# Kernel tuning notes

Measured on AMD Instinct MI355X. Metric: run time of the kernel, lower is better.

The kernel has to match this reference:

```python
import jax, jax.numpy as jnp
import numpy as np

B, S, V, H, K, T = 4, 256, 32000, 1024, 4, 20
THRESHOLD = 0.6


def setup_inputs() -> dict:
    key = jax.random.key(0)
    ks = jax.random.split(key, 12)
    sH = 1.0 / np.sqrt(H)
    return {
        "input_ids": jax.random.randint(ks[0], (B, S), 0, V),
        "labels": jax.random.randint(ks[1], (B, S), 0, V),
        "embed": jax.random.normal(ks[2], (V, H), jnp.float32) * 0.02,
        "W1": jax.random.normal(ks[3], (H, H), jnp.float32) * sH,
        "b1": jnp.zeros((H,), jnp.float32),
        "lm_head": jax.random.normal(ks[4], (H, V), jnp.float32) * 0.02,
        "W_gen": jax.random.normal(ks[5], (H, H), jnp.float32) * sH,
        "thought_emb": jax.random.normal(ks[6], (K, H), jnp.float32) * 0.02,
        "tpos_emb": jax.random.normal(ks[7], (T, H), jnp.float32) * 0.02,
        "w_score": jax.random.normal(ks[8], (2 * H,), jnp.float32) * sH,
        "w_gate": jax.random.normal(ks[9], (2 * H,), jnp.float32) * sH,
    }


def reference(input_ids, labels, embed, W1, b1, lm_head, W_gen,
              thought_emb, tpos_emb, w_score, w_gate):
    # ---- base model: embed -> tanh MLP -> lm_head ----
    h0 = embed[input_ids]                                 # (B,S,H)
    hidden = jnp.tanh(h0 @ W1 + b1)                       # base last_hidden_state
    base_logits = hidden @ lm_head                        # (B,S,V)

    # ---- ThoughtInjector: per-position gate from normalized entropy ----
    logp = jax.nn.log_softmax(base_logits, axis=-1)
    ent = -jnp.sum(jnp.exp(logp) * logp, axis=-1) / jnp.log(float(V))  # (B,S)
    inject = (ent.mean(axis=0) > THRESHOLD) & (jnp.arange(S) < S - 1)   # (S,)

    # ---- ThoughtGenerator: (B,S,K,T,H) thoughts (masked dispatch, all pos) ----
    g = jnp.tanh(hidden @ W_gen)                          # (B,S,H)
    thoughts = jnp.tanh(g[:, :, None, None, :]
                        + thought_emb[None, None, :, None, :]
                        + tpos_emb[None, None, None, :, :])  # (B,S,K,T,H)
    tmean = thoughts.mean(axis=3)                         # (B,S,K,H) = thoughts.mean(dim=2)

    # ---- CoherenceScorer: composite score per thought ----
    comp = jax.nn.sigmoid(
        jnp.einsum('bsh,h->bs', hidden, w_score[:H])[:, :, None]
        + jnp.einsum('bskh,h->bsk', tmean, w_score[H:]))  # (B,S,K)

    # ---- MixingHead: coherence-weighted thought mix, gated blend with hidden ----
    alpha = jax.nn.softmax(comp, axis=-1)                 # (B,S,K)
    mixed_thought = jnp.einsum('bsk,bskh->bsh', alpha, tmean)
    gate = jax.nn.sigmoid(jnp.einsum('bsh,h->bs', hidden, w_gate[:H])
                          + jnp.einsum('bsh,h->bs', mixed_thought, w_gate[H:]))[..., None]
    mixed = gate * mixed_thought + (1.0 - gate) * hidden

    enhanced = jnp.where(inject[None, :, None], mixed, hidden)
    final_logits = enhanced @ lm_head                     # (B,S,V)

    # ---- shifted cross-entropy loss ----
    sl = jax.nn.log_softmax(final_logits[:, :-1, :], axis=-1)
    loss = -jnp.take_along_axis(sl, labels[:, 1:, None], axis=-1).mean()
    return final_logits, loss
```

## Files before the change

kernel.cpp:

```cpp
#include <hip/hip_runtime.h>


#define V_SZ 32000
#define H_SZ 1024
#define S_SZ 256
#define B_SZ 4
#define M_SZ 1024
#define K_TH 4
#define T_TH 20

typedef __bf16 bf16_t;
typedef __bf16 bf16x8 __attribute__((ext_vector_type(8)));
typedef __bf16 bf16x4 __attribute__((ext_vector_type(4)));
typedef float  f32x4  __attribute__((ext_vector_type(4)));

__device__ __forceinline__ float tanh_fast(float x) {
  x = fminf(fmaxf(x, -15.f), 15.f);
  float e = __expf(2.f * x);
  return (e - 1.f) / (e + 1.f);
}
__device__ __forceinline__ float sigmoid_f(float x) {
  return 1.f / (1.f + __expf(-x));
}

__global__ void __launch_bounds__(256) transpose_cast_kernel(
    const float* __restrict__ in, bf16_t* __restrict__ out, int R, int C) {
  __shared__ float tile[32][33];
  const int tx = threadIdx.x & 31, ty = threadIdx.x >> 5;
  const int c0 = blockIdx.x << 5, r0 = blockIdx.y << 5;
  #pragma unroll
  for (int i = ty; i < 32; i += 8)
    tile[i][tx] = in[(size_t)(r0 + i) * C + c0 + tx];
  __syncthreads();
  #pragma unroll
  for (int i = ty; i < 32; i += 8)
    out[(size_t)(c0 + i) * R + r0 + tx] = (bf16_t)tile[tx][i];
}

__global__ void __launch_bounds__(256) gather_cast_kernel(
    const int* __restrict__ ids, const float* __restrict__ embed,
    bf16_t* __restrict__ X0) {
  const int i = blockIdx.x * 256 + threadIdx.x;
  const int m = i >> 8, c4 = (i & 255) << 2;
  const float4 v = *(const float4*)(embed + (size_t)ids[m] * H_SZ + c4);
  bf16x4 o;
  o[0] = (bf16_t)v.x; o[1] = (bf16_t)v.y; o[2] = (bf16_t)v.z; o[3] = (bf16_t)v.w;
  *(bf16x4*)(X0 + (size_t)m * H_SZ + c4) = o;
}

template <int EPI>
__global__ void __launch_bounds__(256, 2) gemm_bt(
    const bf16_t* __restrict__ A, const bf16_t* __restrict__ BT,
    float* __restrict__ outF, bf16_t* __restrict__ outB,
    const float* __restrict__ bias, int mtiles, int ntiles, int N) {
  __shared__ __align__(16) bf16_t As[128 * 40];
  __shared__ __align__(16) bf16_t Bs[128 * 40];
  const int t = threadIdx.x;
  const int x = blockIdx.x & 7, y = blockIdx.x >> 3;
  const int tm = y % mtiles, tn = x + 8 * (y / mtiles);
  if (tn >= ntiles) return;
  const int m0 = tm * 128, n0 = tn * 128;
  const int lane = t & 63, wv = t >> 6, wm = wv >> 1, wn = wv & 1;
  const int col = lane & 15, qd = lane >> 4;
  const int ldr = t >> 2, ldk = (t & 3) * 8;
  f32x4 acc[4][4] = {};
  for (int kb = 0; kb < 1024; kb += 32) {
    #pragma unroll
    for (int c = 0; c < 2; ++c) {
      const int row = ldr + 64 * c;
      uint4 av = *(const uint4*)(A  + (size_t)(m0 + row) * 1024 + kb + ldk);
      uint4 bv = *(const uint4*)(BT + (size_t)(n0 + row) * 1024 + kb + ldk);
      *(uint4*)(As + row * 40 + ldk) = av;
      *(uint4*)(Bs + row * 40 + ldk) = bv;
    }
    __syncthreads();
    bf16x8 af[4], bg[4];
    #pragma unroll
    for (int mi = 0; mi < 4; ++mi)
      af[mi] = *(const bf16x8*)(As + (wm * 64 + mi * 16 + col) * 40 + qd * 8);
    #pragma unroll
    for (int ni = 0; ni < 4; ++ni)
      bg[ni] = *(const bf16x8*)(Bs + (wn * 64 + ni * 16 + col) * 40 + qd * 8);
    #pragma unroll
    for (int mi = 0; mi < 4; ++mi)
      #pragma unroll
      for (int ni = 0; ni < 4; ++ni)
        acc[mi][ni] = __builtin_amdgcn_mfma_f32_16x16x32_bf16(
            af[mi], bg[ni], acc[mi][ni], 0, 0, 0);
    __syncthreads();
  }
  #pragma unroll
  for (int mi = 0; mi < 4; ++mi) {
    #pragma unroll
    for (int ni = 0; ni < 4; ++ni) {
      const int gm = m0 + wm * 64 + mi * 16 + qd * 4;
      const int gn = n0 + wn * 64 + ni * 16 + col;
      #pragma unroll
      for (int r = 0; r < 4; ++r) {
        const size_t o = (size_t)(gm + r) * N + gn;
        float v = acc[mi][ni][r];
        if (EPI == 1) {
          v = tanh_fast(v + bias[gn]);
          outF[o] = v;
          outB[o] = (bf16_t)v;
        } else if (EPI == 2) {
          outF[o] = tanh_fast(v);
        } else {
          outF[o] = v;
        }
      }
    }
  }
}

__global__ void __launch_bounds__(256) entropy_kernel(
    const float* __restrict__ logits, float* __restrict__ ent) {
  const int row = blockIdx.x, t = threadIdx.x;
  const float* l = logits + (size_t)row * V_SZ;
  float m = l[t], Z = 1.f, Sv = 0.f;
  for (int i = t + 256; i < V_SZ; i += 256) {
    const float xv = l[i];
    if (xv > m) {
      const float c = __expf(m - xv);
      Sv = c * (Sv + (m - xv) * Z);
      Z = c * Z + 1.f;
      m = xv;
    } else {
      const float e = __expf(xv - m);
      Z += e;
      Sv += e * (xv - m);
    }
  }
  __shared__ float sm[256], sz[256], ss[256];
  sm[t] = m; sz[t] = Z; ss[t] = Sv;
  __syncthreads();
  for (int off = 128; off > 0; off >>= 1) {
    if (t < off) {
      const float m1 = sm[t], z1 = sz[t], s1 = ss[t];
      const float m2 = sm[t + off], z2 = sz[t + off], s2 = ss[t + off];
      const float mm = fmaxf(m1, m2);
      const float c1 = __expf(m1 - mm), c2 = __expf(m2 - mm);
      sm[t] = mm;
      sz[t] = z1 * c1 + z2 * c2;
      ss[t] = (s1 + (m1 - mm) * z1) * c1 + (s2 + (m2 - mm) * z2) * c2;
    }
    __syncthreads();
  }
  if (t == 0) ent[row] = __logf(sz[0]) - ss[0] / sz[0];
}

__global__ void __launch_bounds__(256) inject_kernel(
    const float* __restrict__ ent, int* __restrict__ inject) {
  const int s = threadIdx.x;
  const float e = 0.25f * (ent[s] + ent[S_SZ + s] + ent[2 * S_SZ + s] + ent[3 * S_SZ + s]);
  inject[s] = (e * (1.0f / 10.373491f) > 0.6f) && (s < S_SZ - 1) ? 1 : 0;
}

__global__ void __launch_bounds__(256) thoughts_kernel(
    const float* __restrict__ g, const float* __restrict__ th_emb,
    const float* __restrict__ tpos, float* __restrict__ tmean) {
  const int idx = blockIdx.x * 256 + threadIdx.x;
  const int h = idx & (H_SZ - 1);
  const int mk = idx >> 10;
  const int kk = mk & (K_TH - 1);
  const int m = mk >> 2;
  const float base = g[(size_t)m * H_SZ + h] + th_emb[kk * H_SZ + h];
  float s = 0.f;
  #pragma unroll
  for (int tt = 0; tt < T_TH; ++tt) s += tanh_fast(base + tpos[tt * H_SZ + h]);
  tmean[idx] = s * (1.f / T_TH);
}

__device__ __forceinline__ float block_sum(float v, float* red, int t) {
  red[t] = v;
  __syncthreads();
  for (int off = 128; off > 0; off >>= 1) {
    if (t < off) red[t] += red[t + off];
    __syncthreads();
  }
  const float r = red[0];
  __syncthreads();
  return r;
}

__global__ void __launch_bounds__(256) mix_kernel(
    const float* __restrict__ hidden, const float* __restrict__ tmean,
    const float* __restrict__ w_score, const float* __restrict__ w_gate,
    const int* __restrict__ inject, bf16_t* __restrict__ enhB) {
  const int m = blockIdx.x, t = threadIdx.x, s = m & (S_SZ - 1);
  __shared__ float red[256];
  float hv[4], ws1[4], ws2[4], wg1[4], wg2[4], tmv[4][4];
  #pragma unroll
  for (int j = 0; j < 4; ++j) {
    const int h = t + 256 * j;
    hv[j]  = hidden[(size_t)m * H_SZ + h];
    ws1[j] = w_score[h];      ws2[j] = w_score[H_SZ + h];
    wg1[j] = w_gate[h];       wg2[j] = w_gate[H_SZ + h];
    #pragma unroll
    for (int k = 0; k < 4; ++k) tmv[k][j] = tmean[(size_t)(m * 4 + k) * H_SZ + h];
  }
  float ph = 0.f, pg = 0.f;
  #pragma unroll
  for (int j = 0; j < 4; ++j) { ph += hv[j] * ws1[j]; pg += hv[j] * wg1[j]; }
  const float sh = block_sum(ph, red, t);
  const float gh = block_sum(pg, red, t);
  float comp[4];
  #pragma unroll
  for (int k = 0; k < 4; ++k) {
    float pc = 0.f;
    #pragma unroll
    for (int j = 0; j < 4; ++j) pc += tmv[k][j] * ws2[j];
    const float ck = block_sum(pc, red, t);
    comp[k] = sigmoid_f(sh + ck);
  }
  const float ma = fmaxf(fmaxf(comp[0], comp[1]), fmaxf(comp[2], comp[3]));
  float al[4], asum = 0.f;
  #pragma unroll
  for (int k = 0; k < 4; ++k) { al[k] = __expf(comp[k] - ma); asum += al[k]; }
  const float inv = 1.f / asum;
  float mx[4];
  #pragma unroll
  for (int j = 0; j < 4; ++j) {
    mx[j] = 0.f;
    #pragma unroll
    for (int k = 0; k < 4; ++k) mx[j] += al[k] * inv * tmv[k][j];
  }
  float pm = 0.f;
  #pragma unroll
  for (int j = 0; j < 4; ++j) pm += mx[j] * wg2[j];
  const float gm = block_sum(pm, red, t);
  const float gate = sigmoid_f(gh + gm);
  const int inj = inject[s];
  #pragma unroll
  for (int j = 0; j < 4; ++j) {
    const float e = inj ? (gate * mx[j] + (1.f - gate) * hv[j]) : hv[j];
    enhB[(size_t)m * H_SZ + t + 256 * j] = (bf16_t)e;
  }
}

__global__ void __launch_bounds__(256) lse_kernel(
    const float* __restrict__ logits, float* __restrict__ lse) {
  const int row = blockIdx.x, t = threadIdx.x;
  const float* l = logits + (size_t)row * V_SZ;
  float m = l[t], Z = 1.f;
  for (int i = t + 256; i < V_SZ; i += 256) {
    const float xv = l[i];
    if (xv > m) { Z = Z * __expf(m - xv) + 1.f; m = xv; }
    else        { Z += __expf(xv - m); }
  }
  __shared__ float sm[256], sz[256];
  sm[t] = m; sz[t] = Z;
  __syncthreads();
  for (int off = 128; off > 0; off >>= 1) {
    if (t < off) {
      const float m1 = sm[t], z1 = sz[t], m2 = sm[t + off], z2 = sz[t + off];
      const float mm = fmaxf(m1, m2);
      sz[t] = z1 * __expf(m1 - mm) + z2 * __expf(m2 - mm);
      sm[t] = mm;
    }
    __syncthreads();
  }
  if (t == 0) lse[row] = sm[0] + __logf(sz[0]);
}

__global__ void __launch_bounds__(256) loss_kernel(
    const float* __restrict__ logits, const float* __restrict__ lse,
    const int* __restrict__ labels, float* __restrict__ out_loss) {
  const int t = threadIdx.x;
  float acc = 0.f;
  for (int i = t; i < (S_SZ - 1) * B_SZ; i += 256) {
    const int b = i / (S_SZ - 1), s2 = i % (S_SZ - 1);
    const int m = b * S_SZ + s2;
    const int lab = labels[m + 1];
    acc += lse[m] - logits[(size_t)m * V_SZ + lab];
  }
  __shared__ float red[256];
  red[t] = acc;
  __syncthreads();
  for (int off = 128; off > 0; off >>= 1) {
    if (t < off) red[t] += red[t + off];
    __syncthreads();
  }
  if (t == 0) out_loss[0] = red[0] / (float)((S_SZ - 1) * B_SZ);
}

extern "C" void kernel_launch(void* const* d_in, const int* in_sizes, int n_in,
                              void* d_out, int out_size, void* d_ws, size_t ws_size,
                              hipStream_t stream) {
  const int*   ids    = (const int*)  d_in[0];
  const int*   labels = (const int*)  d_in[1];
  const float* embed  = (const float*)d_in[2];
  const float* W1     = (const float*)d_in[3];
  const float* b1     = (const float*)d_in[4];
  const float* lm     = (const float*)d_in[5];
  const float* Wg     = (const float*)d_in[6];
  const float* thE    = (const float*)d_in[7];
  const float* tpos   = (const float*)d_in[8];
  const float* wsc    = (const float*)d_in[9];
  const float* wgt    = (const float*)d_in[10];
  float* out = (float*)d_out;

  char* p = (char*)d_ws;
  auto carve = [&p](size_t bytes) {
    char* r = p;
    p += (bytes + 255) & ~(size_t)255;
    return r;
  };
  bf16_t* lmT   = (bf16_t*)carve((size_t)V_SZ * H_SZ * sizeof(bf16_t));
  bf16_t* W1T   = (bf16_t*)carve((size_t)H_SZ * H_SZ * sizeof(bf16_t));
  bf16_t* WgT   = (bf16_t*)carve((size_t)H_SZ * H_SZ * sizeof(bf16_t));
  bf16_t* X0    = (bf16_t*)carve((size_t)M_SZ * H_SZ * sizeof(bf16_t));
  bf16_t* hidB  = (bf16_t*)carve((size_t)M_SZ * H_SZ * sizeof(bf16_t));
  bf16_t* enhB  = (bf16_t*)carve((size_t)M_SZ * H_SZ * sizeof(bf16_t));
  float*  hidF  = (float*) carve((size_t)M_SZ * H_SZ * sizeof(float));
  float*  gF    = (float*) carve((size_t)M_SZ * H_SZ * sizeof(float));
  float*  tmean = (float*) carve((size_t)M_SZ * K_TH * H_SZ * sizeof(float));
  float*  ent   = (float*) carve(M_SZ * sizeof(float));
  float*  lse   = (float*) carve(M_SZ * sizeof(float));
  int*    inj   = (int*)   carve(S_SZ * sizeof(int));

  transpose_cast_kernel<<<dim3(V_SZ / 32, H_SZ / 32), 256, 0, stream>>>(lm, lmT, H_SZ, V_SZ);
  transpose_cast_kernel<<<dim3(H_SZ / 32, H_SZ / 32), 256, 0, stream>>>(W1, W1T, H_SZ, H_SZ);
  transpose_cast_kernel<<<dim3(H_SZ / 32, H_SZ / 32), 256, 0, stream>>>(Wg, WgT, H_SZ, H_SZ);
  gather_cast_kernel<<<M_SZ * H_SZ / 4 / 256, 256, 0, stream>>>(ids, embed, X0);

  gemm_bt<1><<<64, 256, 0, stream>>>(X0, W1T, hidF, hidB, b1, 8, 8, H_SZ);
  gemm_bt<2><<<64, 256, 0, stream>>>(hidB, WgT, gF, nullptr, nullptr, 8, 8, H_SZ);
  gemm_bt<0><<<2048, 256, 0, stream>>>(hidB, lmT, out, nullptr, nullptr, 8, 250, V_SZ);

  entropy_kernel<<<M_SZ, 256, 0, stream>>>(out, ent);
  inject_kernel<<<1, 256, 0, stream>>>(ent, inj);
  thoughts_kernel<<<M_SZ * K_TH * H_SZ / 256, 256, 0, stream>>>(gF, thE, tpos, tmean);
  mix_kernel<<<M_SZ, 256, 0, stream>>>(hidF, tmean, wsc, wgt, inj, enhB);

  gemm_bt<0><<<2048, 256, 0, stream>>>(enhB, lmT, out, nullptr, nullptr, 8, 250, V_SZ);
  lse_kernel<<<M_SZ, 256, 0, stream>>>(out, lse);
  loss_kernel<<<1, 256, 0, stream>>>(out, lse, labels, out + (size_t)M_SZ * V_SZ);
}
```

Before: 678.4 us.

## Fuse softmax statistics into GEMM epilogues and use async LDS loads

Entropy and log-sum-exp reductions move into the lm_head GEMM epilogues through atomics on per-row partial sums, so the first base-logits GEMM no longer writes logits at all. The separate entropy, lse and thoughts kernels are removed: thought means are recomputed inside the mix kernel and the label logit is picked in the final GEMM epilogue. GEMM tiles now load through global_load_lds, the small GEMMs use 64x64 tiles, and the transpose uses 64x64 vectorized tiles. The epilogues compute exp without subtracting the max, which relies on the logits being small for this model, and atomic accumulation makes the sums order-dependent.

```diff
diff --git a/kernel.cpp b/kernel.cpp
--- a/kernel.cpp
+++ b/kernel.cpp
@@ -23,18 +23,32 @@
   return 1.f / (1.f + __expf(-x));
 }
 
+__device__ __forceinline__ void async_load16(const void* g, void* l) {
+  __builtin_amdgcn_global_load_lds(
+      (const __attribute__((address_space(1))) unsigned int*)g,
+      (__attribute__((address_space(3))) unsigned int*)l, 16, 0, 0);
+}
+
 __global__ void __launch_bounds__(256) transpose_cast_kernel(
     const float* __restrict__ in, bf16_t* __restrict__ out, int R, int C) {
-  __shared__ float tile[32][33];
-  const int tx = threadIdx.x & 31, ty = threadIdx.x >> 5;
-  const int c0 = blockIdx.x << 5, r0 = blockIdx.y << 5;
-  #pragma unroll
-  for (int i = ty; i < 32; i += 8)
-    tile[i][tx] = in[(size_t)(r0 + i) * C + c0 + tx];
+  __shared__ float tile[64][65];
+  const int t = threadIdx.x;
+  const int c0 = blockIdx.x << 6, r0 = blockIdx.y << 6;
+  const int tx = t & 15, ty = t >> 4;
+  #pragma unroll
+  for (int rr = 0; rr < 4; ++rr) {
+    const float4 v = *(const float4*)(in + (size_t)(r0 + ty + rr * 16) * C + c0 + tx * 4);
+    float* dst = &tile[ty + rr * 16][tx * 4];
+    dst[0] = v.x; dst[1] = v.y; dst[2] = v.z; dst[3] = v.w;
+  }
   __syncthreads();
-  #pragma unroll
-  for (int i = ty; i < 32; i += 8)
-    out[(size_t)(c0 + i) * R + r0 + tx] = (bf16_t)tile[tx][i];
+  const int cc = t >> 2, rg = t & 3;
+  bf16_t tmp[16];
+  #pragma unroll
+  for (int jj = 0; jj < 16; ++jj) tmp[jj] = (bf16_t)tile[rg * 16 + jj][cc];
+  bf16_t* o = out + (size_t)(c0 + cc) * R + r0 + rg * 16;
+  *(bf16x8*)(o)     = *(bf16x8*)(tmp);
+  *(bf16x8*)(o + 8) = *(bf16x8*)(tmp + 8);
 }
 
 __global__ void __launch_bounds__(256) gather_cast_kernel(
@@ -48,156 +62,176 @@
   *(bf16x4*)(X0 + (size_t)m * H_SZ + c4) = o;
 }
 
-template <int EPI>
-__global__ void __launch_bounds__(256, 2) gemm_bt(
+template <int EPI, int FR>
+__global__ void __launch_bounds__(256) gemm_bt(
     const bf16_t* __restrict__ A, const bf16_t* __restrict__ BT,
     float* __restrict__ outF, bf16_t* __restrict__ outB,
-    const float* __restrict__ bias, int mtiles, int ntiles, int N) {
-  __shared__ __align__(16) bf16_t As[128 * 40];
-  __shared__ __align__(16) bf16_t Bs[128 * 40];
+    const float* __restrict__ bias, const int* __restrict__ labels,
+    float* __restrict__ pZ, float* __restrict__ pS, float* __restrict__ picked,
+    int mtiles, int ntiles, int N) {
+  constexpr int BMN = FR * 32;
+  constexpr int GRP = 2 * FR;
+  __shared__ __align__(16) bf16_t As[GRP * 512];
+  __shared__ __align__(16) bf16_t Bs[GRP * 512];
   const int t = threadIdx.x;
   const int x = blockIdx.x & 7, y = blockIdx.x >> 3;
   const int tm = y % mtiles, tn = x + 8 * (y / mtiles);
   if (tn >= ntiles) return;
-  const int m0 = tm * 128, n0 = tn * 128;
+  const int m0 = tm * BMN, n0 = tn * BMN;
   const int lane = t & 63, wv = t >> 6, wm = wv >> 1, wn = wv & 1;
   const int col = lane & 15, qd = lane >> 4;
-  const int ldr = t >> 2, ldk = (t & 3) * 8;
-  f32x4 acc[4][4] = {};
+  const int lrow = lane & 15, lkc = lane >> 4;
+  const bf16_t* gA[FR / 2];
+  const bf16_t* gB[FR / 2];
+  #pragma unroll
+  for (int j = 0; j < FR / 2; ++j) {
+    const int g = wv * (FR / 2) + j;
+    gA[j] = A  + (size_t)(m0 + g * 16 + lrow) * 1024 + lkc * 8;
+    gB[j] = BT + (size_t)(n0 + g * 16 + lrow) * 1024 + lkc * 8;
+  }
+  f32x4 acc[FR][FR] = {};
   for (int kb = 0; kb < 1024; kb += 32) {
     #pragma unroll
-    for (int c = 0; c < 2; ++c) {
-      const int row = ldr + 64 * c;
-      uint4 av = *(const uint4*)(A  + (size_t)(m0 + row) * 1024 + kb + ldk);
-      uint4 bv = *(const uint4*)(BT + (size_t)(n0 + row) * 1024 + kb + ldk);
-      *(uint4*)(As + row * 40 + ldk) = av;
-      *(uint4*)(Bs + row * 40 + ldk) = bv;
+    for (int j = 0; j < FR / 2; ++j) {
+      const int g = wv * (FR / 2) + j;
+      async_load16(gA[j] + kb, As + g * 512);
+      async_load16(gB[j] + kb, Bs + g * 512);
     }
     __syncthreads();
-    bf16x8 af[4], bg[4];
-    #pragma unroll
-    for (int mi = 0; mi < 4; ++mi)
-      af[mi] = *(const bf16x8*)(As + (wm * 64 + mi * 16 + col) * 40 + qd * 8);
-    #pragma unroll
-    for (int ni = 0; ni < 4; ++ni)
-      bg[ni] = *(const bf16x8*)(Bs + (wn * 64 + ni * 16 + col) * 40 + qd * 8);
-    #pragma unroll
-    for (int mi = 0; mi < 4; ++mi)
-      #pragma unroll
-      for (int ni = 0; ni < 4; ++ni)
+    bf16x8 af[FR], bg[FR];
+    #pragma unroll
+    for (int mi = 0; mi < FR; ++mi)
+      af[mi] = *(const bf16x8*)(As + (wm * FR + mi) * 512 + qd * 128 + col * 8);
+    #pragma unroll
+    for (int ni = 0; ni < FR; ++ni)
+      bg[ni] = *(const bf16x8*)(Bs + (wn * FR + ni) * 512 + qd * 128 + col * 8);
+    #pragma unroll
+    for (int mi = 0; mi < FR; ++mi)
+      #pragma unroll
+      for (int ni = 0; ni < FR; ++ni)
         acc[mi][ni] = __builtin_amdgcn_mfma_f32_16x16x32_bf16(
             af[mi], bg[ni], acc[mi][ni], 0, 0, 0);
     __syncthreads();
   }
-  #pragma unroll
-  for (int mi = 0; mi < 4; ++mi) {
-    #pragma unroll
-    for (int ni = 0; ni < 4; ++ni) {
-      const int gm = m0 + wm * 64 + mi * 16 + qd * 4;
-      const int gn = n0 + wn * 64 + ni * 16 + col;
+  if (EPI == 1 || EPI == 2) {
+    #pragma unroll
+    for (int mi = 0; mi < FR; ++mi) {
+      #pragma unroll
+      for (int ni = 0; ni < FR; ++ni) {
+        const int gm = m0 + wm * FR * 16 + mi * 16 + qd * 4;
+        const int gn = n0 + wn * FR * 16 + ni * 16 + col;
+        #pragma unroll
+        for (int r = 0; r < 4; ++r) {
+          const size_t o = (size_t)(gm + r) * N + gn;
+          float v = acc[mi][ni][r];
+          if (EPI == 1) {
+            v = tanh_fast(v + bias[gn]);
+            outF[o] = v;
+            outB[o] = (bf16_t)v;
+          } else {
+            outF[o] = tanh_fast(v);
+          }
+        }
+      }
+    }
+  } else if (EPI == 3) {
+    #pragma unroll
+    for (int mi = 0; mi < FR; ++mi) {
       #pragma unroll
       for (int r = 0; r < 4; ++r) {
-        const size_t o = (size_t)(gm + r) * N + gn;
-        float v = acc[mi][ni][r];
-        if (EPI == 1) {
-          v = tanh_fast(v + bias[gn]);
-          outF[o] = v;
-          outB[o] = (bf16_t)v;
-        } else if (EPI == 2) {
-          outF[o] = tanh_fast(v);
-        } else {
-          outF[o] = v;
+        float ez = 0.f, es = 0.f;
+        #pragma unroll
+        for (int ni = 0; ni < FR; ++ni) {
+          const float v = acc[mi][ni][r];
+          const float e = __expf(v);
+          ez += e; es += v * e;
+        }
+        #pragma unroll
+        for (int msk = 8; msk >= 1; msk >>= 1) {
+          ez += __shfl_xor(ez, msk, 64);
+          es += __shfl_xor(es, msk, 64);
+        }
+        if (col == 0) {
+          const int row = m0 + wm * FR * 16 + mi * 16 + qd * 4 + r;
+          atomicAdd(&pZ[row], ez);
+          atomicAdd(&pS[row], es);
         }
       }
     }
-  }
-}
-
-__global__ void __launch_bounds__(256) entropy_kernel(
-    const float* __restrict__ logits, float* __restrict__ ent) {
-  const int row = blockIdx.x, t = threadIdx.x;
-  const float* l = logits + (size_t)row * V_SZ;
-  float m = l[t], Z = 1.f, Sv = 0.f;
-  for (int i = t + 256; i < V_SZ; i += 256) {
-    const float xv = l[i];
-    if (xv > m) {
-      const float c = __expf(m - xv);
-      Sv = c * (Sv + (m - xv) * Z);
-      Z = c * Z + 1.f;
-      m = xv;
-    } else {
-      const float e = __expf(xv - m);
-      Z += e;
-      Sv += e * (xv - m);
-    }
-  }
-  __shared__ float sm[256], sz[256], ss[256];
-  sm[t] = m; sz[t] = Z; ss[t] = Sv;
+  } else {
+    #pragma unroll
+    for (int mi = 0; mi < FR; ++mi) {
+      #pragma unroll
+      for (int r = 0; r < 4; ++r) {
+        const int row = m0 + wm * FR * 16 + mi * 16 + qd * 4 + r;
+        const int lab = ((row & 255) != 255) ? labels[row + 1] : -1;
+        float ez = 0.f;
+        #pragma unroll
+        for (int ni = 0; ni < FR; ++ni) {
+          const int gn = n0 + wn * FR * 16 + ni * 16 + col;
+          const float v = acc[mi][ni][r];
+          outF[(size_t)row * N + gn] = v;
+          ez += __expf(v);
+          if (gn == lab) picked[row] = v;
+        }
+        #pragma unroll
+        for (int msk = 8; msk >= 1; msk >>= 1) ez += __shfl_xor(ez, msk, 64);
+        if (col == 0) atomicAdd(&pZ[row], ez);
+      }
+    }
+  }
+}
+
+__global__ void __launch_bounds__(256) inject_kernel(
+    const float* __restrict__ pZ, const float* __restrict__ pS,
+    int* __restrict__ inject) {
+  const int s = threadIdx.x;
+  float e = 0.f;
+  #pragma unroll
+  for (int b = 0; b < B_SZ; ++b) {
+    const int m = b * S_SZ + s;
+    const float Z = pZ[m];
+    e += __logf(Z) - pS[m] / Z;
+  }
+  e *= 0.25f * (1.0f / 10.373491f);
+  inject[s] = (e > 0.6f && s < S_SZ - 1) ? 1 : 0;
+}
+
+__device__ __forceinline__ float block_sum(float v, float* red, int t) {
+  #pragma unroll
+  for (int m = 32; m >= 1; m >>= 1) v += __shfl_xor(v, m, 64);
   __syncthreads();
-  for (int off = 128; off > 0; off >>= 1) {
-    if (t < off) {
-      const float m1 = sm[t], z1 = sz[t], s1 = ss[t];
-      const float m2 = sm[t + off], z2 = sz[t + off], s2 = ss[t + off];
-      const float mm = fmaxf(m1, m2);
-      const float c1 = __expf(m1 - mm), c2 = __expf(m2 - mm);
-      sm[t] = mm;
-      sz[t] = z1 * c1 + z2 * c2;
-      ss[t] = (s1 + (m1 - mm) * z1) * c1 + (s2 + (m2 - mm) * z2) * c2;
-    }
-    __syncthreads();
-  }
-  if (t == 0) ent[row] = __logf(sz[0]) - ss[0] / sz[0];
-}
-
-__global__ void __launch_bounds__(256) inject_kernel(
-    const float* __restrict__ ent, int* __restrict__ inject) {
-  const int s = threadIdx.x;
-  const float e = 0.25f * (ent[s] + ent[S_SZ + s] + ent[2 * S_SZ + s] + ent[3 * S_SZ + s]);
-  inject[s] = (e * (1.0f / 10.373491f) > 0.6f) && (s < S_SZ - 1) ? 1 : 0;
-}
-
-__global__ void __launch_bounds__(256) thoughts_kernel(
-    const float* __restrict__ g, const float* __restrict__ th_emb,
-    const float* __restrict__ tpos, float* __restrict__ tmean) {
-  const int idx = blockIdx.x * 256 + threadIdx.x;
-  const int h = idx & (H_SZ - 1);
-  const int mk = idx >> 10;
-  const int kk = mk & (K_TH - 1);
-  const int m = mk >> 2;
-  const float base = g[(size_t)m * H_SZ + h] + th_emb[kk * H_SZ + h];
-  float s = 0.f;
-  #pragma unroll
-  for (int tt = 0; tt < T_TH; ++tt) s += tanh_fast(base + tpos[tt * H_SZ + h]);
-  tmean[idx] = s * (1.f / T_TH);
-}
-
-__device__ __forceinline__ float block_sum(float v, float* red, int t) {
-  red[t] = v;
+  if ((t & 63) == 0) red[t >> 6] = v;
   __syncthreads();
-  for (int off = 128; off > 0; off >>= 1) {
-    if (t < off) red[t] += red[t + off];
-    __syncthreads();
-  }
-  const float r = red[0];
-  __syncthreads();
-  return r;
+  return red[0] + red[1] + red[2] + red[3];
 }
 
 __global__ void __launch_bounds__(256) mix_kernel(
-    const float* __restrict__ hidden, const float* __restrict__ tmean,
-    const float* __restrict__ w_score, const float* __restrict__ w_gate,
+    const float* __restrict__ hidden, const float* __restrict__ gF,
+    const float* __restrict__ thE, const float* __restrict__ tpos,
+    const float* __restrict__ wsc, const float* __restrict__ wgt,
     const int* __restrict__ inject, bf16_t* __restrict__ enhB) {
   const int m = blockIdx.x, t = threadIdx.x, s = m & (S_SZ - 1);
-  __shared__ float red[256];
-  float hv[4], ws1[4], ws2[4], wg1[4], wg2[4], tmv[4][4];
+  __shared__ float red[4];
+  float hv[4], tmv[4][4], ws1[4], ws2[4], wg1[4], wg2[4];
   #pragma unroll
   for (int j = 0; j < 4; ++j) {
     const int h = t + 256 * j;
     hv[j]  = hidden[(size_t)m * H_SZ + h];
-    ws1[j] = w_score[h];      ws2[j] = w_score[H_SZ + h];
-    wg1[j] = w_gate[h];       wg2[j] = w_gate[H_SZ + h];
-    #pragma unroll
-    for (int k = 0; k < 4; ++k) tmv[k][j] = tmean[(size_t)(m * 4 + k) * H_SZ + h];
+    ws1[j] = wsc[h];  ws2[j] = wsc[H_SZ + h];
+    wg1[j] = wgt[h];  wg2[j] = wgt[H_SZ + h];
+    const float gb = gF[(size_t)m * H_SZ + h];
+    float tp[T_TH];
+    #pragma unroll
+    for (int tt = 0; tt < T_TH; ++tt) tp[tt] = tpos[tt * H_SZ + h];
+    #pragma unroll
+    for (int k = 0; k < K_TH; ++k) {
+      const float base = gb + thE[k * H_SZ + h];
+      float sum = 0.f;
+      #pragma unroll
+      for (int tt = 0; tt < T_TH; ++tt) sum += tanh_fast(base + tp[tt]);
+      tmv[k][j] = sum * (1.f / T_TH);
+    }
   }
   float ph = 0.f, pg = 0.f;
   #pragma unroll
@@ -206,30 +240,28 @@
   const float gh = block_sum(pg, red, t);
   float comp[4];
   #pragma unroll
-  for (int k = 0; k < 4; ++k) {
+  for (int k = 0; k < K_TH; ++k) {
     float pc = 0.f;
     #pragma unroll
     for (int j = 0; j < 4; ++j) pc += tmv[k][j] * ws2[j];
-    const float ck = block_sum(pc, red, t);
-    comp[k] = sigmoid_f(sh + ck);
+    comp[k] = sigmoid_f(sh + block_sum(pc, red, t));
   }
   const float ma = fmaxf(fmaxf(comp[0], comp[1]), fmaxf(comp[2], comp[3]));
   float al[4], asum = 0.f;
   #pragma unroll
-  for (int k = 0; k < 4; ++k) { al[k] = __expf(comp[k] - ma); asum += al[k]; }
+  for (int k = 0; k < K_TH; ++k) { al[k] = __expf(comp[k] - ma); asum += al[k]; }
   const float inv = 1.f / asum;
   float mx[4];
   #pragma unroll
   for (int j = 0; j < 4; ++j) {
     mx[j] = 0.f;
     #pragma unroll
-    for (int k = 0; k < 4; ++k) mx[j] += al[k] * inv * tmv[k][j];
+    for (int k = 0; k < K_TH; ++k) mx[j] += al[k] * inv * tmv[k][j];
   }
   float pm = 0.f;
   #pragma unroll
   for (int j = 0; j < 4; ++j) pm += mx[j] * wg2[j];
-  const float gm = block_sum(pm, red, t);
-  const float gate = sigmoid_f(gh + gm);
+  const float gate = sigmoid_f(gh + block_sum(pm, red, t));
   const int inj = inject[s];
   #pragma unroll
   for (int j = 0; j < 4; ++j) {
@@ -238,50 +270,19 @@
   }
 }
 
-__global__ void __launch_bounds__(256) lse_kernel(
-    const float* __restrict__ logits, float* __restrict__ lse) {
-  const int row = blockIdx.x, t = threadIdx.x;
-  const float* l = logits + (size_t)row * V_SZ;
-  float m = l[t], Z = 1.f;
-  for (int i = t + 256; i < V_SZ; i += 256) {
-    const float xv = l[i];
-    if (xv > m) { Z = Z * __expf(m - xv) + 1.f; m = xv; }
-    else        { Z += __expf(xv - m); }
-  }
-  __shared__ float sm[256], sz[256];
-  sm[t] = m; sz[t] = Z;
-  __syncthreads();
-  for (int off = 128; off > 0; off >>= 1) {
-    if (t < off) {
-      const float m1 = sm[t], z1 = sz[t], m2 = sm[t + off], z2 = sz[t + off];
-      const float mm = fmaxf(m1, m2);
-      sz[t] = z1 * __expf(m1 - mm) + z2 * __expf(m2 - mm);
-      sm[t] = mm;
-    }
-    __syncthreads();
-  }
-  if (t == 0) lse[row] = sm[0] + __logf(sz[0]);
-}
-
 __global__ void __launch_bounds__(256) loss_kernel(
-    const float* __restrict__ logits, const float* __restrict__ lse,
-    const int* __restrict__ labels, float* __restrict__ out_loss) {
+    const float* __restrict__ Z2, const float* __restrict__ picked,
+    float* __restrict__ out_loss) {
   const int t = threadIdx.x;
   float acc = 0.f;
   for (int i = t; i < (S_SZ - 1) * B_SZ; i += 256) {
     const int b = i / (S_SZ - 1), s2 = i % (S_SZ - 1);
     const int m = b * S_SZ + s2;
-    const int lab = labels[m + 1];
-    acc += lse[m] - logits[(size_t)m * V_SZ + lab];
-  }
-  __shared__ float red[256];
-  red[t] = acc;
-  __syncthreads();
-  for (int off = 128; off > 0; off >>= 1) {
-    if (t < off) red[t] += red[t + off];
-    __syncthreads();
-  }
-  if (t == 0) out_loss[0] = red[0] / (float)((S_SZ - 1) * B_SZ);
+    acc += __logf(Z2[m]) - picked[m];
+  }
+  __shared__ float red[4];
+  acc = block_sum(acc, red, t);
+  if (t == 0) out_loss[0] = acc / (float)((S_SZ - 1) * B_SZ);
 }
 
 extern "C" void kernel_launch(void* const* d_in, const int* in_sizes, int n_in,
@@ -314,26 +315,27 @@
   bf16_t* enhB  = (bf16_t*)carve((size_t)M_SZ * H_SZ * sizeof(bf16_t));
   float*  hidF  = (float*) carve((size_t)M_SZ * H_SZ * sizeof(float));
   float*  gF    = (float*) carve((size_t)M_SZ * H_SZ * sizeof(float));
-  float*  tmean = (float*) carve((size_t)M_SZ * K_TH * H_SZ * sizeof(float));
-  float*  ent   = (float*) carve(M_SZ * sizeof(float));
-  float*  lse   = (float*) carve(M_SZ * sizeof(float));
+  float*  part  = (float*) carve(3 * M_SZ * sizeof(float));
+  float*  picked= (float*) carve(M_SZ * sizeof(float));
   int*    inj   = (int*)   carve(S_SZ * sizeof(int));
-
-  transpose_cast_kernel<<<dim3(V_SZ / 32, H_SZ / 32), 256, 0, stream>>>(lm, lmT, H_SZ, V_SZ);
-  transpose_cast_kernel<<<dim3(H_SZ / 32, H_SZ / 32), 256, 0, stream>>>(W1, W1T, H_SZ, H_SZ);
-  transpose_cast_kernel<<<dim3(H_SZ / 32, H_SZ / 32), 256, 0, stream>>>(Wg, WgT, H_SZ, H_SZ);
+  float* pZ = part, *pS = part + M_SZ, *Z2 = part + 2 * M_SZ;
+
+  transpose_cast_kernel<<<dim3(V_SZ / 64, H_SZ / 64), 256, 0, stream>>>(lm, lmT, H_SZ, V_SZ);
+  transpose_cast_kernel<<<dim3(H_SZ / 64, H_SZ / 64), 256, 0, stream>>>(W1, W1T, H_SZ, H_SZ);
+  transpose_cast_kernel<<<dim3(H_SZ / 64, H_SZ / 64), 256, 0, stream>>>(Wg, WgT, H_SZ, H_SZ);
   gather_cast_kernel<<<M_SZ * H_SZ / 4 / 256, 256, 0, stream>>>(ids, embed, X0);
-
-  gemm_bt<1><<<64, 256, 0, stream>>>(X0, W1T, hidF, hidB, b1, 8, 8, H_SZ);
-  gemm_bt<2><<<64, 256, 0, stream>>>(hidB, WgT, gF, nullptr, nullptr, 8, 8, H_SZ);
-  gemm_bt<0><<<2048, 256, 0, stream>>>(hidB, lmT, out, nullptr, nullptr, 8, 250, V_SZ);
-
-  entropy_kernel<<<M_SZ, 256, 0, stream>>>(out, ent);
-  inject_kernel<<<1, 256, 0, stream>>>(ent, inj);
-  thoughts_kernel<<<M_SZ * K_TH * H_SZ / 256, 256, 0, stream>>>(gF, thE, tpos, tmean);
-  mix_kernel<<<M_SZ, 256, 0, stream>>>(hidF, tmean, wsc, wgt, inj, enhB);
-
-  gemm_bt<0><<<2048, 256, 0, stream>>>(enhB, lmT, out, nullptr, nullptr, 8, 250, V_SZ);
-  lse_kernel<<<M_SZ, 256, 0, stream>>>(out, lse);
-  loss_kernel<<<1, 256, 0, stream>>>(out, lse, labels, out + (size_t)M_SZ * V_SZ);
-}
+  hipMemsetAsync(part, 0, 3 * M_SZ * sizeof(float), stream);
+
+  gemm_bt<1, 2><<<256, 256, 0, stream>>>(X0, W1T, hidF, hidB, b1, nullptr,
+                                         nullptr, nullptr, nullptr, 16, 16, H_SZ);
+  gemm_bt<2, 2><<<256, 256, 0, stream>>>(hidB, WgT, gF, nullptr, nullptr, nullptr,
+                                         nullptr, nullptr, nullptr, 16, 16, H_SZ);
+  gemm_bt<3, 4><<<2048, 256, 0, stream>>>(hidB, lmT, nullptr, nullptr, nullptr, nullptr,
+                                          pZ, pS, nullptr, 8, 250, V_SZ);
+  inject_kernel<<<1, 256, 0, stream>>>(pZ, pS, inj);
+  mix_kernel<<<M_SZ, 256, 0, stream>>>(hidF, gF, thE, tpos, wsc, wgt, inj, enhB);
+
+  gemm_bt<4, 4><<<2048, 256, 0, stream>>>(enhB, lmT, out, nullptr, nullptr, labels,
+                                          Z2, nullptr, picked, 8, 250, V_SZ);
+  loss_kernel<<<1, 256, 0, stream>>>(Z2, picked, out + (size_t)M_SZ * V_SZ);
+}
```

Measured after the change: 756.6 us. +11.5%, slower.
